# Kernel optimization log

Hardware: AMD Instinct MI355X
Metric: run time of the kernel (lower is better)

The kernel has to match this reference:

```python
import jax, jax.numpy as jnp
from jax import lax
import numpy as np

NPOINT, RADIUS, NSAMPLE = 2048, 0.2, 32
EPS = 1e-5


def fps(xyz, npoint):
    # furthest point sampling; xyz [B,N,3] -> idx [B,npoint] int32
    B, N, _ = xyz.shape

    def body(carry, _):
        dist, far = carry  # dist [B,N], far [B]
        centroid = jnp.take_along_axis(xyz, far[:, None, None], axis=1)  # [B,1,3]
        d = jnp.sum((xyz - centroid) ** 2, -1)  # [B,N]
        dist = jnp.minimum(dist, d)
        nxt = jnp.argmax(dist, -1).astype(jnp.int32)
        return (dist, nxt), far

    init = (jnp.full((B, N), 1e10, xyz.dtype), jnp.zeros((B,), jnp.int32))
    _, idx = lax.scan(body, init, None, length=npoint)
    return jnp.transpose(idx)  # [B, npoint]


def ball_query(radius, nsample, xyz, new_xyz):
    # xyz [B,N,3], new_xyz [B,S,3] -> idx [B,S,nsample] int32
    B, N, _ = xyz.shape
    sqr = jnp.sum((new_xyz[:, :, None, :] - xyz[:, None, :, :]) ** 2, -1)  # [B,S,N]
    idx = jnp.broadcast_to(jnp.arange(N, dtype=jnp.int32), sqr.shape)
    idx = jnp.where(sqr > radius * radius, N, idx)
    idx = jnp.sort(idx, -1)[:, :, :nsample]  # first nsample in-ball indices
    first = idx[:, :, :1]
    return jnp.where(idx == N, first, idx)  # pad misses with first hit


def group(x, idx):
    # x [B,N,C], idx [B,S,K] -> [B,S,K,C]
    return jax.vmap(lambda xb, ib: xb[ib])(x, idx)


def setup_inputs() -> dict:
    key = jax.random.key(0)
    ks = jax.random.split(key, 8)
    B, N = 8, 8192
    mlp, in_c = [32, 32, 64], 6
    inp = {
        'xyz': jax.random.normal(ks[0], (B, N, 3), jnp.float32),
        'points': jax.random.normal(ks[1], (B, N, 3), jnp.float32),
    }
    cin = in_c
    for i, cout in enumerate(mlp):
        inp[f'w{i}'] = jax.random.normal(ks[2 + i], (cout, cin), jnp.float32) * (1.0 / np.sqrt(cin))
        inp[f'b{i}'] = jnp.zeros((cout,), jnp.float32)
        inp[f'g{i}'] = jnp.ones((cout,), jnp.float32)
        inp[f'be{i}'] = jnp.zeros((cout,), jnp.float32)
        cin = cout
    return inp


def reference(xyz, points, w0, b0, g0, be0, w1, b1, g1, be1, w2, b2, g2, be2):
    fps_idx = fps(xyz, NPOINT)
    new_xyz = jax.vmap(lambda xb, ib: xb[ib])(xyz, fps_idx)  # [B,S,3]
    idx = ball_query(RADIUS, NSAMPLE, xyz, new_xyz)  # [B,S,K]
    grouped_xyz = group(xyz, idx) - new_xyz[:, :, None, :]  # [B,S,K,3]
    feat = jnp.concatenate([grouped_xyz, group(points, idx)], -1)  # [B,S,K,6]
    for w, b, g, be in ((w0, b0, g0, be0), (w1, b1, g1, be1), (w2, b2, g2, be2)):
        feat = jnp.einsum('bskc,oc->bsko', feat, w) + b  # 1x1 conv
        mean = jnp.mean(feat, axis=(0, 1, 2))
        var = jnp.var(feat, axis=(0, 1, 2))
        feat = (feat - mean) * lax.rsqrt(var + EPS) * g + be  # BN (train stats)
        feat = jax.nn.relu(feat)
    new_points = jnp.max(feat, axis=2)  # max over neighborhood -> [B,S,64]
    return new_xyz, new_points
```

## Files before the change

kernel.cpp:

```cpp
#include <hip/hip_runtime.h>
#include <math.h>

#define BB 8
#define NN 8192
#define SS 2048
#define KK 32
#define NP (BB*SS*KK)
#define EPSF 1e-5f

template <int CTRL>
__device__ __forceinline__ unsigned long long dpp_max_step(unsigned long long key) {
    unsigned lo = (unsigned)key, hi = (unsigned)(key >> 32);
    unsigned nlo = (unsigned)__builtin_amdgcn_update_dpp((int)lo, (int)lo, CTRL, 0xf, 0xf, false);
    unsigned nhi = (unsigned)__builtin_amdgcn_update_dpp((int)hi, (int)hi, CTRL, 0xf, 0xf, false);
    unsigned long long nk = ((unsigned long long)nhi << 32) | nlo;
    return nk > key ? nk : key;
}

__device__ __forceinline__ unsigned long long wave_max_u64(unsigned long long key) {
    key = dpp_max_step<0x111>(key);
    key = dpp_max_step<0x112>(key);
    key = dpp_max_step<0x114>(key);
    key = dpp_max_step<0x118>(key);
    key = dpp_max_step<0x142>(key);
    key = dpp_max_step<0x143>(key);
    return key;
}

__global__ __launch_bounds__(512) void fps_kernel(const float* __restrict__ xyz,
                                                  float* __restrict__ out_newxyz) {
    const int T = 512;
    const int PPT = NN / T;
    int b = blockIdx.x;
    int t = threadIdx.x;
    int wid  = t >> 6;
    int lane = t & 63;
    const float* x = xyz + b * NN * 3;
    float* nout = out_newxyz + b * SS * 3;

    __shared__ float4 lxyz[NN];
    __shared__ unsigned long long skey[2][8];

    float px[PPT], py[PPT], pz[PPT], dist[PPT];
#pragma unroll
    for (int i = 0; i < PPT; i++) {
        int p = t + i * T;
        float vx = x[p * 3 + 0];
        float vy = x[p * 3 + 1];
        float vz = x[p * 3 + 2];
        px[i] = vx; py[i] = vy; pz[i] = vz;
        lxyz[p] = make_float4(vx, vy, vz, 0.f);
        dist[i] = 1e10f;
    }
    __syncthreads();
    float4 c0 = lxyz[0];
    float cx = c0.x, cy = c0.y, cz = c0.z;

    for (int it = 0; it < SS; it++) {
        if (t == 0) {
            nout[it * 3 + 0] = cx;
            nout[it * 3 + 1] = cy;
            nout[it * 3 + 2] = cz;
        }
        float lmax = -1.0f;
        int   li   = 0;
#pragma unroll
        for (int i = 0; i < PPT; i++) {
            float dx = __fsub_rn(px[i], cx);
            float dy = __fsub_rn(py[i], cy);
            float dz = __fsub_rn(pz[i], cz);
            float d  = __fadd_rn(__fadd_rn(__fmul_rn(dx, dx), __fmul_rn(dy, dy)),
                                 __fmul_rn(dz, dz));
            float dd = fminf(dist[i], d);
            dist[i] = dd;
            bool gt = dd > lmax;
            lmax = gt ? dd : lmax;
            li   = gt ? i  : li;
        }
        int p = t + (li << 9);
        unsigned long long key =
            ((unsigned long long)__float_as_uint(lmax) << 32) | (unsigned)(~p);
        key = wave_max_u64(key);
        if (lane == 63) skey[it & 1][wid] = key;
        __syncthreads();
        unsigned long long k = skey[it & 1][0];
#pragma unroll
        for (int j = 1; j < 8; j++) {
            unsigned long long o = skey[it & 1][j];
            k = (o > k) ? o : k;
        }
        int gi = (int)(~(unsigned)k) & (NN - 1);
        float4 c = lxyz[gi];
        cx = c.x; cy = c.y; cz = c.z;
    }
}

__global__ __launch_bounds__(256) void ballq_kernel(const float* __restrict__ xyz,
                                                    const float* __restrict__ new_xyz,
                                                    int* __restrict__ idx_out) {
    int q    = blockIdx.x * 4 + (threadIdx.x >> 6);
    int lane = threadIdx.x & 63;
    int b    = q >> 11;
    const float* x = xyz + b * NN * 3;
    const float* c = new_xyz + q * 3;
    float cx = c[0], cy = c[1], cz = c[2];
    int* out = idx_out + q * KK;
    const float R2 = (float)(0.2 * 0.2);

    int count = 0;
    int first = -1;
    for (int base = 0; base < NN; base += 64) {
        int p = base + lane;
        float dx = __fsub_rn(x[p * 3 + 0], cx);
        float dy = __fsub_rn(x[p * 3 + 1], cy);
        float dz = __fsub_rn(x[p * 3 + 2], cz);
        float d  = __fadd_rn(__fadd_rn(__fmul_rn(dx, dx), __fmul_rn(dy, dy)),
                             __fmul_rn(dz, dz));
        bool in = !(d > R2);
        unsigned long long m = __ballot(in);
        if (first < 0 && m != 0ull) first = base + __ffsll((unsigned long long)m) - 1;
        int pre = __popcll(m & ((1ull << lane) - 1ull));
        int pos = count + pre;
        if (in && pos < KK) out[pos] = p;
        count += __popcll(m);
        if (count >= KK) break;
    }
    for (int i2 = count + lane; i2 < KK; i2 += 64) out[i2] = first;
}

__device__ __forceinline__ void load_in6(const float* __restrict__ xyz,
                                         const float* __restrict__ points,
                                         const float* __restrict__ new_xyz,
                                         const int* __restrict__ idx, int p, float inx[6]) {
    int bs = p >> 5;
    int b  = bs >> 11;
    int pt = idx[p];
    const float* xb = xyz + ((long)b * NN + pt) * 3;
    const float* pb = points + ((long)b * NN + pt) * 3;
    const float* nx = new_xyz + bs * 3;
    inx[0] = xb[0] - nx[0];
    inx[1] = xb[1] - nx[1];
    inx[2] = xb[2] - nx[2];
    inx[3] = pb[0];
    inx[4] = pb[1];
    inx[5] = pb[2];
}

template <int CIN, int COUT>
__device__ __forceinline__ void linear(const float* __restrict__ w,
                                       const float* __restrict__ bias,
                                       const float* xin, float* yout) {
#pragma unroll
    for (int o = 0; o < COUT; o++) {
        float acc = bias[o];
#pragma unroll
        for (int j = 0; j < CIN; j++) acc = fmaf(w[o * CIN + j], xin[j], acc);
        yout[o] = acc;
    }
}

template <int C>
__device__ __forceinline__ void bn_coef(const float* __restrict__ stats,
                                        const float* __restrict__ g,
                                        const float* __restrict__ be,
                                        float* s_sc, float* s_sh) {
    int t = threadIdx.x;
    if (t < C) {
        float mean = stats[t] * (1.0f / (float)NP);
        float var  = stats[C + t] * (1.0f / (float)NP) - mean * mean;
        float rstd = 1.0f / sqrtf(var + EPSF);
        float sc = g[t] * rstd;
        s_sc[t] = sc;
        s_sh[t] = be[t] - mean * sc;
    }
    __syncthreads();
}

template <int C>
__device__ __forceinline__ void accum_stats(const float* y, float* __restrict__ gstats) {
    __shared__ float buf[256][33];
    int t = threadIdx.x;
#pragma unroll
    for (int h = 0; h < C / 32; h++) {
        __syncthreads();
#pragma unroll
        for (int c = 0; c < 32; c++) buf[t][c] = y[h * 32 + c];
        __syncthreads();
        if (t < 32) {
            float s = 0.f, sq = 0.f;
            for (int r = 0; r < 256; r++) {
                float v = buf[r][t];
                s += v;
                sq = fmaf(v, v, sq);
            }
            atomicAdd(&gstats[h * 32 + t], s);
            atomicAdd(&gstats[C + h * 32 + t], sq);
        }
    }
}

__global__ __launch_bounds__(256) void l0_stats_kernel(
    const float* __restrict__ xyz, const float* __restrict__ points,
    const float* __restrict__ new_xyz, const int* __restrict__ idx,
    const float* __restrict__ w0, const float* __restrict__ b0_,
    float* __restrict__ stats0) {
    int p = blockIdx.x * 256 + threadIdx.x;
    float inx[6];
    load_in6(xyz, points, new_xyz, idx, p, inx);
    float y0[32];
    linear<6, 32>(w0, b0_, inx, y0);
    accum_stats<32>(y0, stats0);
}

__global__ __launch_bounds__(256) void l1_stats_kernel(
    const float* __restrict__ xyz, const float* __restrict__ points,
    const float* __restrict__ new_xyz, const int* __restrict__ idx,
    const float* __restrict__ w0, const float* __restrict__ b0_,
    const float* __restrict__ g0, const float* __restrict__ be0,
    const float* __restrict__ w1, const float* __restrict__ b1_,
    const float* __restrict__ stats0, float* __restrict__ stats1) {
    __shared__ float sc0[32], sh0[32];
    bn_coef<32>(stats0, g0, be0, sc0, sh0);
    int p = blockIdx.x * 256 + threadIdx.x;
    float inx[6];
    load_in6(xyz, points, new_xyz, idx, p, inx);
    float y0[32];
    linear<6, 32>(w0, b0_, inx, y0);
#pragma unroll
    for (int c = 0; c < 32; c++) y0[c] = fmaxf(fmaf(y0[c], sc0[c], sh0[c]), 0.f);
    float y1[32];
    linear<32, 32>(w1, b1_, y0, y1);
    accum_stats<32>(y1, stats1);
}

__global__ __launch_bounds__(256) void l2_stats_kernel(
    const float* __restrict__ xyz, const float* __restrict__ points,
    const float* __restrict__ new_xyz, const int* __restrict__ idx,
    const float* __restrict__ w0, const float* __restrict__ b0_,
    const float* __restrict__ g0, const float* __restrict__ be0,
    const float* __restrict__ w1, const float* __restrict__ b1_,
    const float* __restrict__ g1, const float* __restrict__ be1,
    const float* __restrict__ w2, const float* __restrict__ b2_,
    const float* __restrict__ stats0, const float* __restrict__ stats1,
    float* __restrict__ stats2) {
    __shared__ float sc0[32], sh0[32], sc1[32], sh1[32];
    bn_coef<32>(stats0, g0, be0, sc0, sh0);
    bn_coef<32>(stats1, g1, be1, sc1, sh1);
    int p = blockIdx.x * 256 + threadIdx.x;
    float inx[6];
    load_in6(xyz, points, new_xyz, idx, p, inx);
    float y0[32];
    linear<6, 32>(w0, b0_, inx, y0);
#pragma unroll
    for (int c = 0; c < 32; c++) y0[c] = fmaxf(fmaf(y0[c], sc0[c], sh0[c]), 0.f);
    float y1[32];
    linear<32, 32>(w1, b1_, y0, y1);
#pragma unroll
    for (int c = 0; c < 32; c++) y1[c] = fmaxf(fmaf(y1[c], sc1[c], sh1[c]), 0.f);
    float y2[64];
    linear<32, 64>(w2, b2_, y1, y2);
    accum_stats<64>(y2, stats2);
}

__global__ __launch_bounds__(256) void final_kernel(
    const float* __restrict__ xyz, const float* __restrict__ points,
    const float* __restrict__ new_xyz, const int* __restrict__ idx,
    const float* __restrict__ w0, const float* __restrict__ b0_,
    const float* __restrict__ g0, const float* __restrict__ be0,
    const float* __restrict__ w1, const float* __restrict__ b1_,
    const float* __restrict__ g1, const float* __restrict__ be1,
    const float* __restrict__ w2, const float* __restrict__ b2_,
    const float* __restrict__ g2, const float* __restrict__ be2,
    const float* __restrict__ stats0, const float* __restrict__ stats1,
    const float* __restrict__ stats2, float* __restrict__ out_points) {
    __shared__ float sc0[32], sh0[32], sc1[32], sh1[32], sc2[64], sh2[64];
    bn_coef<32>(stats0, g0, be0, sc0, sh0);
    bn_coef<32>(stats1, g1, be1, sc1, sh1);
    bn_coef<64>(stats2, g2, be2, sc2, sh2);
    int p = blockIdx.x * 256 + threadIdx.x;
    float inx[6];
    load_in6(xyz, points, new_xyz, idx, p, inx);
    float y0[32];
    linear<6, 32>(w0, b0_, inx, y0);
#pragma unroll
    for (int c = 0; c < 32; c++) y0[c] = fmaxf(fmaf(y0[c], sc0[c], sh0[c]), 0.f);
    float y1[32];
    linear<32, 32>(w1, b1_, y0, y1);
#pragma unroll
    for (int c = 0; c < 32; c++) y1[c] = fmaxf(fmaf(y1[c], sc1[c], sh1[c]), 0.f);
    float y2[64];
    linear<32, 64>(w2, b2_, y1, y2);
#pragma unroll
    for (int c = 0; c < 64; c++) {
        float v = fmaxf(fmaf(y2[c], sc2[c], sh2[c]), 0.f);
#pragma unroll
        for (int off = 1; off < 32; off <<= 1)
            v = fmaxf(v, __shfl_xor(v, off));
        y2[c] = v;
    }
    int lane = threadIdx.x & 63;
    if ((lane & 31) == 0) {
        int bs = p >> 5;
        float4* o = (float4*)(out_points + (long)bs * 64);
#pragma unroll
        for (int c4 = 0; c4 < 16; c4++)
            o[c4] = make_float4(y2[c4 * 4], y2[c4 * 4 + 1], y2[c4 * 4 + 2], y2[c4 * 4 + 3]);
    }
}

extern "C" void kernel_launch(void* const* d_in, const int* in_sizes, int n_in,
                              void* d_out, int out_size, void* d_ws, size_t ws_size,
                              hipStream_t stream) {
    (void)in_sizes; (void)n_in; (void)out_size; (void)ws_size;
    const float* xyz    = (const float*)d_in[0];
    const float* points = (const float*)d_in[1];
    const float* w0  = (const float*)d_in[2];
    const float* b0_ = (const float*)d_in[3];
    const float* g0  = (const float*)d_in[4];
    const float* be0 = (const float*)d_in[5];
    const float* w1  = (const float*)d_in[6];
    const float* b1_ = (const float*)d_in[7];
    const float* g1  = (const float*)d_in[8];
    const float* be1 = (const float*)d_in[9];
    const float* w2  = (const float*)d_in[10];
    const float* b2_ = (const float*)d_in[11];
    const float* g2  = (const float*)d_in[12];
    const float* be2 = (const float*)d_in[13];

    float* out        = (float*)d_out;
    float* out_newxyz = out;
    float* out_points = out + BB * SS * 3;

    int*   idx    = (int*)d_ws;
    float* stats  = (float*)d_ws + NP;
    float* stats0 = stats;
    float* stats1 = stats + 64;
    float* stats2 = stats + 128;

    hipMemsetAsync(stats, 0, 256 * sizeof(float), stream);

    fps_kernel<<<BB, 512, 0, stream>>>(xyz, out_newxyz);
    ballq_kernel<<<BB * SS / 4, 256, 0, stream>>>(xyz, out_newxyz, idx);
    l0_stats_kernel<<<NP / 256, 256, 0, stream>>>(xyz, points, out_newxyz, idx, w0, b0_, stats0);
    l1_stats_kernel<<<NP / 256, 256, 0, stream>>>(xyz, points, out_newxyz, idx,
                                                  w0, b0_, g0, be0, w1, b1_, stats0, stats1);
    l2_stats_kernel<<<NP / 256, 256, 0, stream>>>(xyz, points, out_newxyz, idx,
                                                  w0, b0_, g0, be0, w1, b1_, g1, be1,
                                                  w2, b2_, stats0, stats1, stats2);
    final_kernel<<<NP / 256, 256, 0, stream>>>(xyz, points, out_newxyz, idx,
                                               w0, b0_, g0, be0, w1, b1_, g1, be1,
                                               w2, b2_, g2, be2, stats0, stats1, stats2,
                                               out_points);
}
```

Measured before the change: 2.389 ms.

## Spatially sort points into grid tiles and skip FPS tiles by bounding-box pruning

FPS now bins points into an 8x8x8 grid, reorders them in LDS by cell, and builds 64-point tiles with bounding boxes. Each iteration updates only tiles whose box could lie closer to the new centroid than that tile's current maximum distance, and keeps a per-tile max key with original-index tie-breaking. The aim is to avoid recomputing all 8192 distances per step in the serial FPS loop. The cost is 256 threads instead of 512, all state held in LDS rather than registers, data-dependent loops that diverge per wave, and an extra barrier per iteration.

New measurement: 5.095 ms. 113% more time.

```diff
diff --git a/kernel.cpp b/kernel.cpp
--- a/kernel.cpp
+++ b/kernel.cpp
@@ -27,10 +27,9 @@
     return key;
 }
 
-__global__ __launch_bounds__(512) void fps_kernel(const float* __restrict__ xyz,
+__global__ __launch_bounds__(256) void fps_kernel(const float* __restrict__ xyz,
                                                   float* __restrict__ out_newxyz) {
-    const int T = 512;
-    const int PPT = NN / T;
+#pragma clang fp contract(off)
     int b = blockIdx.x;
     int t = threadIdx.x;
     int wid  = t >> 6;
@@ -38,23 +37,92 @@
     const float* x = xyz + b * NN * 3;
     float* nout = out_newxyz + b * SS * 3;
 
-    __shared__ float4 lxyz[NN];
-    __shared__ unsigned long long skey[2][8];
-
-    float px[PPT], py[PPT], pz[PPT], dist[PPT];
-#pragma unroll
-    for (int i = 0; i < PPT; i++) {
-        int p = t + i * T;
-        float vx = x[p * 3 + 0];
-        float vy = x[p * 3 + 1];
-        float vz = x[p * 3 + 2];
-        px[i] = vx; py[i] = vy; pz[i] = vz;
-        lxyz[p] = make_float4(vx, vy, vz, 0.f);
-        dist[i] = 1e10f;
-    }
-    __syncthreads();
-    float4 c0 = lxyz[0];
-    float cx = c0.x, cy = c0.y, cz = c0.z;
+    __shared__ float sx[NN], sy[NN], sz[NN];
+    __shared__ unsigned short sidx[NN];
+    __shared__ float sdist[NN];
+    __shared__ float tbox[128][6];
+    __shared__ __align__(16) unsigned long long tkey[128];
+    __shared__ int cellstart[512];
+    __shared__ float red[4][6];
+    __shared__ int spos0;
+
+    float mnx = 1e30f, mxx = -1e30f, mny = 1e30f, mxy = -1e30f, mnz = 1e30f, mxz = -1e30f;
+    for (int i = 0; i < NN / 256; i++) {
+        int p = t + i * 256;
+        float px = x[p * 3 + 0], py = x[p * 3 + 1], pz = x[p * 3 + 2];
+        mnx = fminf(mnx, px); mxx = fmaxf(mxx, px);
+        mny = fminf(mny, py); mxy = fmaxf(mxy, py);
+        mnz = fminf(mnz, pz); mxz = fmaxf(mxz, pz);
+    }
+#pragma unroll
+    for (int off = 1; off < 64; off <<= 1) {
+        mnx = fminf(mnx, __shfl_xor(mnx, off)); mxx = fmaxf(mxx, __shfl_xor(mxx, off));
+        mny = fminf(mny, __shfl_xor(mny, off)); mxy = fmaxf(mxy, __shfl_xor(mxy, off));
+        mnz = fminf(mnz, __shfl_xor(mnz, off)); mxz = fmaxf(mxz, __shfl_xor(mxz, off));
+    }
+    if (lane == 0) {
+        red[wid][0] = mnx; red[wid][1] = mxx; red[wid][2] = mny;
+        red[wid][3] = mxy; red[wid][4] = mnz; red[wid][5] = mxz;
+    }
+    __syncthreads();
+    mnx = fminf(fminf(red[0][0], red[1][0]), fminf(red[2][0], red[3][0]));
+    mxx = fmaxf(fmaxf(red[0][1], red[1][1]), fmaxf(red[2][1], red[3][1]));
+    mny = fminf(fminf(red[0][2], red[1][2]), fminf(red[2][2], red[3][2]));
+    mxy = fmaxf(fmaxf(red[0][3], red[1][3]), fmaxf(red[2][3], red[3][3]));
+    mnz = fminf(fminf(red[0][4], red[1][4]), fminf(red[2][4], red[3][4]));
+    mxz = fmaxf(fmaxf(red[0][5], red[1][5]), fmaxf(red[2][5], red[3][5]));
+    float sclx = 8.0f / (mxx - mnx), scly = 8.0f / (mxy - mny), sclz = 8.0f / (mxz - mnz);
+
+    cellstart[t] = 0; cellstart[t + 256] = 0;
+    __syncthreads();
+    for (int i = 0; i < NN / 256; i++) {
+        int p = t + i * 256;
+        float px = x[p * 3 + 0], py = x[p * 3 + 1], pz = x[p * 3 + 2];
+        int ix = min(7, max(0, (int)((px - mnx) * sclx)));
+        int iy = min(7, max(0, (int)((py - mny) * scly)));
+        int iz = min(7, max(0, (int)((pz - mnz) * sclz)));
+        atomicAdd(&cellstart[(iz * 8 + iy) * 8 + ix], 1);
+    }
+    __syncthreads();
+    if (t == 0) {
+        int run = 0;
+        for (int c2 = 0; c2 < 512; c2++) { int v = cellstart[c2]; cellstart[c2] = run; run += v; }
+    }
+    __syncthreads();
+    for (int i = 0; i < NN / 256; i++) {
+        int p = t + i * 256;
+        float px = x[p * 3 + 0], py = x[p * 3 + 1], pz = x[p * 3 + 2];
+        int ix = min(7, max(0, (int)((px - mnx) * sclx)));
+        int iy = min(7, max(0, (int)((py - mny) * scly)));
+        int iz = min(7, max(0, (int)((pz - mnz) * sclz)));
+        int pos = atomicAdd(&cellstart[(iz * 8 + iy) * 8 + ix], 1);
+        sx[pos] = px; sy[pos] = py; sz[pos] = pz;
+        sidx[pos] = (unsigned short)p;
+        if (p == 0) spos0 = pos;
+        sdist[p] = 1e10f;
+    }
+    if (t < 128) tkey[t] = ((unsigned long long)__float_as_uint(1e10f)) << 32;
+    __syncthreads();
+    for (int tt = 0; tt < 32; tt++) {
+        int tile = wid * 32 + tt;
+        int q = tile * 64 + lane;
+        float vx = sx[q], vy = sy[q], vz = sz[q];
+        float ax = vx, bx2 = vx, ay = vy, by2 = vy, az = vz, bz2 = vz;
+#pragma unroll
+        for (int off = 1; off < 64; off <<= 1) {
+            ax = fminf(ax, __shfl_xor(ax, off)); bx2 = fmaxf(bx2, __shfl_xor(bx2, off));
+            ay = fminf(ay, __shfl_xor(ay, off)); by2 = fmaxf(by2, __shfl_xor(by2, off));
+            az = fminf(az, __shfl_xor(az, off)); bz2 = fmaxf(bz2, __shfl_xor(bz2, off));
+        }
+        if (lane == 0) {
+            tbox[tile][0] = ax; tbox[tile][1] = bx2; tbox[tile][2] = ay;
+            tbox[tile][3] = by2; tbox[tile][4] = az; tbox[tile][5] = bz2;
+        }
+    }
+    __syncthreads();
+
+    int sc = spos0;
+    float cx = sx[sc], cy = sy[sc], cz = sz[sc];
 
     for (int it = 0; it < SS; it++) {
         if (t == 0) {
@@ -62,36 +130,50 @@
             nout[it * 3 + 1] = cy;
             nout[it * 3 + 2] = cz;
         }
-        float lmax = -1.0f;
-        int   li   = 0;
-#pragma unroll
-        for (int i = 0; i < PPT; i++) {
-            float dx = __fsub_rn(px[i], cx);
-            float dy = __fsub_rn(py[i], cy);
-            float dz = __fsub_rn(pz[i], cz);
+        bool dirty = false;
+        if (lane < 32) {
+            int tile = wid * 32 + lane;
+            float t1 = __fsub_rn(tbox[tile][0], cx);
+            float t2 = __fsub_rn(cx, tbox[tile][1]);
+            float tx = fmaxf(fmaxf(t1, t2), 0.f);
+            t1 = __fsub_rn(tbox[tile][2], cy);
+            t2 = __fsub_rn(cy, tbox[tile][3]);
+            float ty = fmaxf(fmaxf(t1, t2), 0.f);
+            t1 = __fsub_rn(tbox[tile][4], cz);
+            t2 = __fsub_rn(cz, tbox[tile][5]);
+            float tz = fmaxf(fmaxf(t1, t2), 0.f);
+            float dmin = __fadd_rn(__fadd_rn(__fmul_rn(tx, tx), __fmul_rn(ty, ty)),
+                                   __fmul_rn(tz, tz));
+            float tmax = __uint_as_float((unsigned)(tkey[tile] >> 32));
+            dirty = dmin < tmax;
+        }
+        unsigned long long m = __ballot(dirty);
+        while (m) {
+            int bb = __ffsll(m) - 1;
+            m &= m - 1;
+            int tile = wid * 32 + bb;
+            int q = tile * 64 + lane;
+            float dx = __fsub_rn(sx[q], cx);
+            float dy = __fsub_rn(sy[q], cy);
+            float dz = __fsub_rn(sz[q], cz);
             float d  = __fadd_rn(__fadd_rn(__fmul_rn(dx, dx), __fmul_rn(dy, dy)),
                                  __fmul_rn(dz, dz));
-            float dd = fminf(dist[i], d);
-            dist[i] = dd;
-            bool gt = dd > lmax;
-            lmax = gt ? dd : lmax;
-            li   = gt ? i  : li;
-        }
-        int p = t + (li << 9);
-        unsigned long long key =
-            ((unsigned long long)__float_as_uint(lmax) << 32) | (unsigned)(~p);
-        key = wave_max_u64(key);
-        if (lane == 63) skey[it & 1][wid] = key;
+            float e = fminf(sdist[q], d);
+            sdist[q] = e;
+            unsigned orig = sidx[q];
+            unsigned long long key = ((unsigned long long)__float_as_uint(e) << 32)
+                                   | ((8191u - orig) << 13) | (unsigned)q;
+            key = wave_max_u64(key);
+            if (lane == 63) tkey[tile] = key;
+        }
         __syncthreads();
-        unsigned long long k = skey[it & 1][0];
-#pragma unroll
-        for (int j = 1; j < 8; j++) {
-            unsigned long long o = skey[it & 1][j];
-            k = (o > k) ? o : k;
-        }
-        int gi = (int)(~(unsigned)k) & (NN - 1);
-        float4 c = lxyz[gi];
-        cx = c.x; cy = c.y; cz = c.z;
+        ulonglong2 kp = *(const ulonglong2*)&tkey[lane * 2];
+        unsigned long long k = kp.x > kp.y ? kp.x : kp.y;
+        k = wave_max_u64(k);
+        k = __shfl(k, 63);
+        __syncthreads();
+        int gs = (int)((unsigned)k & 0x1FFFu);
+        cx = sx[gs]; cy = sy[gs]; cz = sz[gs];
     }
 }
 
@@ -339,7 +421,7 @@
 
     hipMemsetAsync(stats, 0, 256 * sizeof(float), stream);
 
-    fps_kernel<<<BB, 512, 0, stream>>>(xyz, out_newxyz);
+    fps_kernel<<<BB, 256, 0, stream>>>(xyz, out_newxyz);
     ballq_kernel<<<BB * SS / 4, 256, 0, stream>>>(xyz, out_newxyz, idx);
     l0_stats_kernel<<<NP / 256, 256, 0, stream>>>(xyz, points, out_newxyz, idx, w0, b0_, stats0);
     l1_stats_kernel<<<NP / 256, 256, 0, stream>>>(xyz, points, out_newxyz, idx,
```

## Shrink FPS block to 256 threads with split max chains and fused stats zeroing

Applied to the files above, without the earlier changes.

The FPS kernel now runs 256 threads per block, so each thread owns 32 points and only 4 wave keys are combined per iteration, which cuts cross-wave reduction and barrier cost on this strictly serial loop. The per-thread argmax is split into four independent fmax chains, with a second pass that recovers the index by comparing against the stored distances, so the dependent compare-select chain is shorter. The 4 wave keys are read with two 16-byte shared loads, and the stats memset is folded into the FPS kernel to drop one launch. In exchange each thread carries more registers and serial work per iteration, and equal-distance ties now pick the lowest local slot, which should still match the expected lowest index.

Result: no change. 2.405 ms (+0.6%).

```diff
diff --git a/kernel.cpp b/kernel.cpp
--- a/kernel.cpp
+++ b/kernel.cpp
@@ -7,6 +7,7 @@
 #define KK 32
 #define NP (BB*SS*KK)
 #define EPSF 1e-5f
+#define TT 256
 
 template <int CTRL>
 __device__ __forceinline__ unsigned long long dpp_max_step(unsigned long long key) {
@@ -27,10 +28,11 @@
     return key;
 }
 
-__global__ __launch_bounds__(512) void fps_kernel(const float* __restrict__ xyz,
-                                                  float* __restrict__ out_newxyz) {
-    const int T = 512;
-    const int PPT = NN / T;
+__global__ __launch_bounds__(TT) void fps_kernel(const float* __restrict__ xyz,
+                                                 float* __restrict__ out_newxyz,
+                                                 float* __restrict__ stats) {
+#pragma clang fp contract(off)
+    const int PPT = NN / TT;
     int b = blockIdx.x;
     int t = threadIdx.x;
     int wid  = t >> 6;
@@ -39,18 +41,18 @@
     float* nout = out_newxyz + b * SS * 3;
 
     __shared__ float4 lxyz[NN];
-    __shared__ unsigned long long skey[2][8];
+    __shared__ __align__(16) unsigned long long skey[2][4];
 
     float px[PPT], py[PPT], pz[PPT], dist[PPT];
 #pragma unroll
-    for (int i = 0; i < PPT; i++) {
-        int p = t + i * T;
+    for (int j = 0; j < PPT; j++) {
+        int p = t + j * TT;
         float vx = x[p * 3 + 0];
         float vy = x[p * 3 + 1];
         float vz = x[p * 3 + 2];
-        px[i] = vx; py[i] = vy; pz[i] = vz;
+        px[j] = vx; py[j] = vy; pz[j] = vz;
         lxyz[p] = make_float4(vx, vy, vz, 0.f);
-        dist[i] = 1e10f;
+        dist[j] = 1e10f;
     }
     __syncthreads();
     float4 c0 = lxyz[0];
@@ -62,37 +64,44 @@
             nout[it * 3 + 1] = cy;
             nout[it * 3 + 2] = cz;
         }
-        float lmax = -1.0f;
-        int   li   = 0;
-#pragma unroll
-        for (int i = 0; i < PPT; i++) {
-            float dx = __fsub_rn(px[i], cx);
-            float dy = __fsub_rn(py[i], cy);
-            float dz = __fsub_rn(pz[i], cz);
+        float m0 = -1.0f, m1 = -1.0f, m2 = -1.0f, m3 = -1.0f;
+#pragma unroll
+        for (int j = 0; j < PPT; j++) {
+            float dx = __fsub_rn(px[j], cx);
+            float dy = __fsub_rn(py[j], cy);
+            float dz = __fsub_rn(pz[j], cz);
             float d  = __fadd_rn(__fadd_rn(__fmul_rn(dx, dx), __fmul_rn(dy, dy)),
                                  __fmul_rn(dz, dz));
-            float dd = fminf(dist[i], d);
-            dist[i] = dd;
-            bool gt = dd > lmax;
-            lmax = gt ? dd : lmax;
-            li   = gt ? i  : li;
+            float e = fminf(dist[j], d);
+            dist[j] = e;
+            if ((j & 3) == 0)      m0 = fmaxf(m0, e);
+            else if ((j & 3) == 1) m1 = fmaxf(m1, e);
+            else if ((j & 3) == 2) m2 = fmaxf(m2, e);
+            else                   m3 = fmaxf(m3, e);
         }
-        int p = t + (li << 9);
+        float lmax = fmaxf(fmaxf(m0, m1), fmaxf(m2, m3));
+        int li = 0;
+#pragma unroll
+        for (int j = PPT - 1; j >= 0; j--)
+            li = (dist[j] == lmax) ? j : li;
+        int p = t + (li << 8);
         unsigned long long key =
             ((unsigned long long)__float_as_uint(lmax) << 32) | (unsigned)(~p);
         key = wave_max_u64(key);
         if (lane == 63) skey[it & 1][wid] = key;
         __syncthreads();
-        unsigned long long k = skey[it & 1][0];
-#pragma unroll
-        for (int j = 1; j < 8; j++) {
-            unsigned long long o = skey[it & 1][j];
-            k = (o > k) ? o : k;
-        }
+        const ulonglong2* sk = (const ulonglong2*)&skey[it & 1][0];
+        ulonglong2 ab = sk[0];
+        ulonglong2 cd = sk[1];
+        unsigned long long k = ab.x;
+        k = (ab.y > k) ? ab.y : k;
+        k = (cd.x > k) ? cd.x : k;
+        k = (cd.y > k) ? cd.y : k;
         int gi = (int)(~(unsigned)k) & (NN - 1);
         float4 c = lxyz[gi];
         cx = c.x; cy = c.y; cz = c.z;
     }
+    if (b == 0) stats[t] = 0.f;
 }
 
 __global__ __launch_bounds__(256) void ballq_kernel(const float* __restrict__ xyz,
@@ -337,9 +346,7 @@
     float* stats1 = stats + 64;
     float* stats2 = stats + 128;
 
-    hipMemsetAsync(stats, 0, 256 * sizeof(float), stream);
-
-    fps_kernel<<<BB, 512, 0, stream>>>(xyz, out_newxyz);
+    fps_kernel<<<BB, TT, 0, stream>>>(xyz, out_newxyz, stats);
     ballq_kernel<<<BB * SS / 4, 256, 0, stream>>>(xyz, out_newxyz, idx);
     l0_stats_kernel<<<NP / 256, 256, 0, stream>>>(xyz, points, out_newxyz, idx, w0, b0_, stats0);
     l1_stats_kernel<<<NP / 256, 256, 0, stream>>>(xyz, points, out_newxyz, idx,
```
